# Optimization experiments

Measured on AMD Instinct MI355X. Metric: run time of the kernel, lower is better.

## Reference

```python
import jax, jax.numpy as jnp
import numpy as np

MO = 48          # max_output_len (positional slots)
D = 32           # d_inner
NA = 8           # n_actions
STOP = 0
CAT_PRIM, CAT_MOD, CAT_COMB = 0, 1, 2


def _mlp(feats, w1, b1, w2, b2, w3, b3):
    # Linear -> GELU(exact, erf) -> Linear -> GELU -> Linear (torch nn.GELU default is exact)
    h = jax.nn.gelu(feats @ w1.T + b1, approximate=False)
    h = jax.nn.gelu(h @ w2.T + b2, approximate=False)
    return h @ w3.T + b3


def setup_inputs() -> dict:
    key = jax.random.key(0)
    ks = jax.random.split(key, 20)
    B, N = 1024, 16
    inp = {
        'node_cats': jax.random.randint(ks[0], (B, N), 0, 3, dtype=jnp.int32),
        'node_subs': jax.random.randint(ks[1], (B, N), 0, 2, dtype=jnp.int32),
        'node_mask': jax.random.randint(ks[2], (B, N), 0, 2, dtype=jnp.int32),
        'child_left': jax.random.randint(ks[3], (B, N), 0, N, dtype=jnp.int32),
        'child_right': jax.random.randint(ks[4], (B, N), 0, N, dtype=jnp.int32),
        'action_embed': jax.random.normal(ks[5], (NA, D), jnp.float32),
        'mod_w1': jax.random.normal(ks[6], (128, 3), jnp.float32) * 0.1,
        'mod_b1': jax.random.normal(ks[7], (128,), jnp.float32) * 0.02,
        'mod_w2': jax.random.normal(ks[8], (128, 128), jnp.float32) * 0.05,
        'mod_b2': jax.random.normal(ks[9], (128,), jnp.float32) * 0.02,
        'mod_w3': jax.random.normal(ks[10], (MO * MO, 128), jnp.float32) * 0.01,
        'mod_b3': (4.0 * jnp.eye(MO)).flatten(),  # identity-ish init as in torch code
        'comb_w1': jax.random.normal(ks[11], (128, 4), jnp.float32) * 0.1,
        'comb_b1': jax.random.normal(ks[12], (128,), jnp.float32) * 0.02,
        'comb_w2': jax.random.normal(ks[13], (128, 128), jnp.float32) * 0.05,
        'comb_b2': jax.random.normal(ks[14], (128,), jnp.float32) * 0.02,
        'comb_w3': jax.random.normal(ks[15], (MO * 2 * MO, 128), jnp.float32) * 0.01,
        'comb_b3': (4.0 * jnp.eye(MO, 2 * MO)).flatten(),
    }
    return inp


def _forward(node_cats, node_subs, node_mask, child_left, child_right,
             action_embed, mod_w1, mod_b1, mod_w2, mod_b2, mod_w3, mod_b3,
             comb_w1, comb_b1, comb_w2, comb_b2, comb_w3, comb_b3):
    B, N = node_cats.shape
    mask = node_mask.astype(bool)
    cl = jnp.clip(child_left, 0, N - 1)
    cr = jnp.clip(child_right, 0, N - 1)
    prim_mask = (node_cats == CAT_PRIM) & mask
    mod_mask = (node_cats == CAT_MOD) & mask
    comb_mask = (node_cats == CAT_COMB) & mask
    subs01 = jnp.clip(node_subs, 0, 1)
    sub_oh = jax.nn.one_hot(subs01, 2, dtype=jnp.float32)  # (B,N,2)

    # --- primitive init: buffer[0] = action_embed[subs+1], zeros elsewhere ---
    action_ids = jnp.clip(node_subs + 1, 0, NA - 1)
    prim_vecs = action_embed[action_ids]  # (B,N,D)
    buffers = jnp.zeros((B, N, MO, D), jnp.float32)
    buffers = buffers.at[:, :, 0, :].set(prim_vecs * prim_mask[..., None].astype(jnp.float32))
    counts = prim_mask.astype(jnp.float32)  # (B,N)

    # --- modifier stage ---
    child_buf = jnp.take_along_axis(buffers, cl[:, :, None, None], axis=1)  # (B,N,MO,D)
    child_cnt = jnp.take_along_axis(counts, cl, axis=1)  # (B,N)
    feats = jnp.concatenate([child_cnt[..., None] / MO, sub_oh], axis=-1)  # (B,N,3)
    logits = _mlp(feats, mod_w1, mod_b1, mod_w2, mod_b2, mod_w3, mod_b3).reshape(B, N, MO, MO)
    attn = jax.nn.softmax(logits, axis=-1)
    mod_buf = jnp.einsum('bnpq,bnqd->bnpd', attn, child_buf)
    factors = jnp.array([2.0, 3.0], jnp.float32)[subs01]
    mod_cnt = jnp.minimum(child_cnt * factors, float(MO))
    buffers = jnp.where(mod_mask[:, :, None, None], mod_buf, buffers)
    counts = jnp.where(mod_mask, mod_cnt, counts)

    # --- combinator stage ---
    left_buf = jnp.take_along_axis(buffers, cl[:, :, None, None], axis=1)
    right_buf = jnp.take_along_axis(buffers, cr[:, :, None, None], axis=1)
    left_cnt = jnp.take_along_axis(counts, cl, axis=1)
    right_cnt = jnp.take_along_axis(counts, cr, axis=1)
    feats = jnp.concatenate([left_cnt[..., None] / MO, right_cnt[..., None] / MO, sub_oh], axis=-1)  # (B,N,4)
    logits = _mlp(feats, comb_w1, comb_b1, comb_w2, comb_b2, comb_w3, comb_b3).reshape(B, N, MO, 2 * MO)
    attn = jax.nn.softmax(logits, axis=-1)
    concat_buf = jnp.concatenate([left_buf, right_buf], axis=2)  # (B,N,2MO,D)
    comb_buf = jnp.einsum('bnpq,bnqd->bnpd', attn, concat_buf)
    comb_cnt = jnp.minimum(left_cnt + right_cnt, float(MO))
    buffers = jnp.where(comb_mask[:, :, None, None], comb_buf, buffers)
    counts = jnp.where(comb_mask, comb_cnt, counts)

    # --- decode root with tied embedding + stop bias ---
    root_buf = buffers[:, 0, :, :]  # (B,MO,D)
    out = jnp.einsum('bpd,ad->bpa', root_buf, action_embed)  # (B,MO,NA)
    positions = jnp.arange(MO, dtype=jnp.float32)[None, :]  # (1,MO)
    is_stop = (positions >= counts[:, 0:1]).astype(jnp.float32)[..., None]  # (B,MO,1)
    stop_bias = jnp.zeros((NA,), jnp.float32).at[STOP].set(8.0)
    return out + is_stop * stop_bias


def reference(node_cats, node_subs, node_mask, child_left, child_right,
              action_embed, mod_w1, mod_b1, mod_w2, mod_b2, mod_w3, mod_b3,
              comb_w1, comb_b1, comb_w2, comb_b2, comb_w3, comb_b3):
    return _forward(node_cats, node_subs, node_mask, child_left, child_right,
                    action_embed, mod_w1, mod_b1, mod_w2, mod_b2, mod_w3, mod_b3,
                    comb_w1, comb_b1, comb_w2, comb_b2, comb_w3, comb_b3)
```

## Files before the change

### kernel.cpp

```cpp
#include <hip/hip_runtime.h>
#include <hip/hip_bf16.h>
#include <float.h>


#define NNODE 16

#define MODCOL_OFF 0
#define C0_OFF     192
#define C48_OFF    1728
#define DOTL_OFF   3264
#define DOTR_OFF   9408
#define G_OFF      15552
#define H2_OFF     15616

__device__ __forceinline__ float gelu_exact(float x) {
    return 0.5f * x * (1.0f + erff(x * 0.70710678118654752f));
}

__device__ __forceinline__ float dot128(const float* __restrict__ w,
                                        const float* __restrict__ h) {
    const float4* w4 = (const float4*)w;
    float s = 0.f;
    #pragma unroll
    for (int i = 0; i < 32; ++i) {
        float4 v = w4[i];
        s += v.x * h[4 * i + 0] + v.y * h[4 * i + 1] +
             v.z * h[4 * i + 2] + v.w * h[4 * i + 3];
    }
    return s;
}

__global__ __launch_bounds__(128) void scan_tables_a(
    const float* __restrict__ E,
    const float* __restrict__ mw1, const float* __restrict__ mb1,
    const float* __restrict__ mw2, const float* __restrict__ mb2,
    const float* __restrict__ mw3, const float* __restrict__ mb3,
    const float* __restrict__ cw1, const float* __restrict__ cb1,
    const float* __restrict__ cw2, const float* __restrict__ cb2,
    float* __restrict__ ws)
{
    __shared__ float h1[128];
    __shared__ float h2s[128];
    __shared__ float lg[48];

    const int tid = threadIdx.x;
    const int blk = blockIdx.x;

    if (blk < 192) {
        const int m = blk / 48, p = blk % 48;
        const int cnt = m >> 1, sub = m & 1;
        const float f0 = (float)cnt / 48.0f;
        const float f1 = (sub == 0) ? 1.0f : 0.0f;
        const float f2 = (sub == 1) ? 1.0f : 0.0f;
        h1[tid] = gelu_exact(mw1[tid * 3 + 0] * f0 + mw1[tid * 3 + 1] * f1 +
                             mw1[tid * 3 + 2] * f2 + mb1[tid]);
        __syncthreads();
        h2s[tid] = gelu_exact(dot128(mw2 + tid * 128, h1) + mb2[tid]);
        __syncthreads();
        if (tid < 48)
            lg[tid] = dot128(mw3 + (p * 48 + tid) * 128, h2s) + mb3[p * 48 + tid];
        __syncthreads();
        if (tid == 0) {
            float mx = lg[0];
            for (int q = 1; q < 48; ++q) mx = fmaxf(mx, lg[q]);
            float s = 0.f;
            for (int q = 0; q < 48; ++q) s += expf(lg[q] - mx);
            ws[MODCOL_OFF + m * 48 + p] = expf(lg[0] - mx) / s;
        }
        return;
    }
    if (blk < 224) {
        const int c = blk - 192;
        const int csub = c & 1;
        const int rc = (c >> 1) & 3;
        const int lc = (c >> 3) & 3;
        const float f0 = (float)lc / 48.0f;
        const float f1 = (float)rc / 48.0f;
        const float f2 = (csub == 0) ? 1.0f : 0.0f;
        const float f3 = (csub == 1) ? 1.0f : 0.0f;
        h1[tid] = gelu_exact(cw1[tid * 4 + 0] * f0 + cw1[tid * 4 + 1] * f1 +
                             cw1[tid * 4 + 2] * f2 + cw1[tid * 4 + 3] * f3 + cb1[tid]);
        __syncthreads();
        ws[H2_OFF + c * 128 + tid] =
            gelu_exact(dot128(cw2 + tid * 128, h1) + cb2[tid]);
        return;
    }
    if (tid < 64) {
        const int i = tid >> 3, a = tid & 7;
        float s = 0.f;
        #pragma unroll
        for (int d = 0; d < 32; ++d) s += E[i * 32 + d] * E[a * 32 + d];
        ws[G_OFF + tid] = s;
    }
}

__global__ __launch_bounds__(128, 4) void scan_tables_b(
    const float* __restrict__ cw3, const float* __restrict__ cb3,
    float* __restrict__ ws)
{
    __shared__ float h2s[128];
    __shared__ float mc[192];
    __shared__ float lg[96];
    __shared__ float pr[96];
    __shared__ float red[4];

    const int tid = threadIdx.x;
    const int p = blockIdx.x >> 5;
    const int c = blockIdx.x & 31;

    h2s[tid] = ws[H2_OFF + c * 128 + tid];
    for (int i = tid; i < 192; i += 128) mc[i] = ws[MODCOL_OFF + i];
    __syncthreads();

    const int j = tid & 3;
    const int rbase = tid >> 2;
    const float4* h24 = (const float4*)h2s;
    #pragma unroll
    for (int o = 0; o < 3; ++o) {
        const int r = o * 32 + rbase;
        const float4* w4 = (const float4*)(cw3 + (p * 96 + r) * 128);
        float s = 0.f;
        #pragma unroll
        for (int i = 0; i < 8; ++i) {
            const int f4i = i * 4 + j;
            float4 w = w4[f4i];
            float4 h = h24[f4i];
            s += w.x * h.x + w.y * h.y + w.z * h.z + w.w * h.w;
        }
        s += __shfl_xor(s, 1);
        s += __shfl_xor(s, 2);
        if (j == 0) lg[r] = s;
    }
    __syncthreads();

    const int wv = tid >> 6;
    float lv = (tid < 96) ? (lg[tid] + cb3[p * 96 + tid]) : -FLT_MAX;
    float m = lv;
    #pragma unroll
    for (int d = 32; d > 0; d >>= 1) m = fmaxf(m, __shfl_xor(m, d));
    if ((tid & 63) == 0) red[wv] = m;
    __syncthreads();
    const float mx = fmaxf(red[0], red[1]);

    float ev = (tid < 96) ? expf(lv - mx) : 0.f;
    if (tid < 96) pr[tid] = ev;
    float sum = ev;
    #pragma unroll
    for (int d = 32; d > 0; d >>= 1) sum += __shfl_xor(sum, d);
    if ((tid & 63) == 0) red[2 + wv] = sum;
    __syncthreads();
    const float inv = 1.0f / (red[2] + red[3]);

    if (tid == 0) {
        ws[C0_OFF + c * 48 + p]  = pr[0]  * inv;
        ws[C48_OFF + c * 48 + p] = pr[48] * inv;
    }
    if (tid < 8) {
        const int mm = tid & 3;
        const int side = tid >> 2;
        const float* q0 = pr + side * 48;
        const float* mr = mc + mm * 48;
        float s = 0.f;
        #pragma unroll
        for (int q = 0; q < 48; ++q) s += q0[q] * mr[q];
        const int off = (side == 0 ? DOTL_OFF : DOTR_OFF) + (c * 4 + mm) * 48 + p;
        ws[off] = s * inv;
    }
}

__global__ __launch_bounds__(384) void scan_output(
    const int* __restrict__ cats, const int* __restrict__ subs,
    const int* __restrict__ mask, const int* __restrict__ cl,
    const int* __restrict__ cr,
    const float* __restrict__ ws,
    float* __restrict__ out)
{
    __shared__ int sc[NNODE], ss[NNODE], sm[NNODE], sl[NNODE], sr[NNODE];
    __shared__ int s_dec[7];
    __shared__ float s_G[64];

    const int b = blockIdx.x;
    const int tid = threadIdx.x;
    if (tid < NNODE) {
        sc[tid] = cats[b * NNODE + tid];
        ss[tid] = subs[b * NNODE + tid];
        sm[tid] = mask[b * NNODE + tid];
        sl[tid] = cl[b * NNODE + tid];
        sr[tid] = cr[b * NNODE + tid];
    } else if (tid >= 64 && tid < 128) {
        s_G[tid - 64] = ws[G_OFF + tid - 64];
    }
    __syncthreads();

    if (tid == 0) {
        auto clampN  = [](int x) { return x < 0 ? 0 : (x > NNODE - 1 ? NNODE - 1 : x); };
        auto clamp01 = [](int x) { return x < 0 ? 0 : (x > 1 ? 1 : x); };
        auto clampA  = [](int x) { return x < 0 ? 0 : (x > 7 ? 7 : x); };
        auto PRIM = [&](int n) { return (sc[n] == 0) && (sm[n] != 0); };
        auto MODM = [&](int n) { return (sc[n] == 1) && (sm[n] != 0); };
        auto AID  = [&](int n) { return clampA(ss[n] + 1); };

        int modeL = 0, modeR = 0, offL = 0, offR = 0, aidL = 0, aidR = 0, count0 = 0;
        const int  cat0 = sc[0];
        const bool msk0 = sm[0] != 0;
        const int  sub0 = clamp01(ss[0]);
        const int  cl0  = clampN(sl[0]);
        const int  cr0  = clampN(sr[0]);

        if (cat0 == 2 && msk0) {
            auto cnt2 = [&](int n) -> int {
                if (MODM(n)) {
                    int c1 = PRIM(clampN(sl[n])) ? 1 : 0;
                    int f  = clamp01(ss[n]) ? 3 : 2;
                    int v  = c1 * f;
                    return v > 48 ? 48 : v;
                }
                return PRIM(n) ? 1 : 0;
            };
            const int l = cl0, r = cr0;
            const int lcc = cnt2(l), rcc = cnt2(r);
            const int cidx = (lcc * 4 + rcc) * 2 + sub0;
            count0 = lcc + rcc; if (count0 > 48) count0 = 48;
            if (MODM(l)) {
                const int g = clampN(sl[l]);
                if (PRIM(g)) {
                    modeL = 1; aidL = AID(g);
                    const int mcfg = 2 + clamp01(ss[l]);
                    offL = DOTL_OFF + (cidx * 4 + mcfg) * 48;
                }
            } else if (PRIM(l)) {
                modeL = 1; aidL = AID(l);
                offL = C0_OFF + cidx * 48;
            }
            if (MODM(r)) {
                const int g = clampN(sl[r]);
                if (PRIM(g)) {
                    modeR = 1; aidR = AID(g);
                    const int mcfg = 2 + clamp01(ss[r]);
                    offR = DOTR_OFF + (cidx * 4 + mcfg) * 48;
                }
            } else if (PRIM(r)) {
                modeR = 1; aidR = AID(r);
                offR = C48_OFF + cidx * 48;
            }
        } else if (cat0 == 1 && msk0) {
            const int ch = cl0;
            const int c1 = PRIM(ch) ? 1 : 0;
            count0 = c1 * (sub0 ? 3 : 2); if (count0 > 48) count0 = 48;
            if (c1) {
                modeL = 1; aidL = AID(ch);
                offL = MODCOL_OFF + (2 + sub0) * 48;
            }
        } else if (cat0 == 0 && msk0) {
            modeL = 2; aidL = AID(0); count0 = 1;
        }
        s_dec[0] = modeL; s_dec[1] = modeR; s_dec[2] = offL; s_dec[3] = offR;
        s_dec[4] = aidL;  s_dec[5] = aidR;  s_dec[6] = count0;
    }
    __syncthreads();

    const int p = tid >> 3, a = tid & 7;
    const int modeL = s_dec[0], modeR = s_dec[1];
    float v = 0.f;
    if (modeL == 1)       v += ws[s_dec[2] + p] * s_G[s_dec[4] * 8 + a];
    else if (modeL == 2)  { if (p == 0) v = s_G[s_dec[4] * 8 + a]; }
    if (modeR == 1)       v += ws[s_dec[3] + p] * s_G[s_dec[5] * 8 + a];
    if (a == 0 && p >= s_dec[6]) v += 8.0f;
    out[b * 384 + tid] = v;
}

extern "C" void kernel_launch(void* const* d_in, const int* in_sizes, int n_in,
                              void* d_out, int out_size, void* d_ws, size_t ws_size,
                              hipStream_t stream) {
    const int* cats = (const int*)d_in[0];
    const int* subs = (const int*)d_in[1];
    const int* mask = (const int*)d_in[2];
    const int* cl   = (const int*)d_in[3];
    const int* cr   = (const int*)d_in[4];
    const float* E   = (const float*)d_in[5];
    const float* mw1 = (const float*)d_in[6];
    const float* mb1 = (const float*)d_in[7];
    const float* mw2 = (const float*)d_in[8];
    const float* mb2 = (const float*)d_in[9];
    const float* mw3 = (const float*)d_in[10];
    const float* mb3 = (const float*)d_in[11];
    const float* cw1 = (const float*)d_in[12];
    const float* cb1 = (const float*)d_in[13];
    const float* cw2 = (const float*)d_in[14];
    const float* cb2 = (const float*)d_in[15];
    const float* cw3 = (const float*)d_in[16];
    const float* cb3 = (const float*)d_in[17];
    float* ws  = (float*)d_ws;
    float* out = (float*)d_out;
    const int B = in_sizes[0] / NNODE;

    scan_tables_a<<<225, 128, 0, stream>>>(E, mw1, mb1, mw2, mb2, mw3, mb3,
                                           cw1, cb1, cw2, cb2, ws);
    scan_tables_b<<<48 * 32, 128, 0, stream>>>(cw3, cb3, ws);
    scan_output<<<B, 384, 0, stream>>>(cats, subs, mask, cl, cr, ws, out);
}
```

Measured before the change: 107.5 us.

## Merge table kernels into one launch and move mod-combine dot into output kernel

Fuses the two table-building kernels into a single launch. Each comb block now recomputes its own first two MLP layers instead of reading them from a prior kernel. Only the mod tables that are needed (count 1) are computed, and the full attention rows are stored to workspace. The mod-column dot product is deferred to the output kernel, which computes it per batch row from the stored attention. This removes one launch and an inter-kernel dependency, in exchange for redundant layer-2 MLP work in 1536 blocks and a larger workspace write plus per-row dot products in the output kernel.

```diff
diff --git a/kernel.cpp b/kernel.cpp
--- a/kernel.cpp
+++ b/kernel.cpp
@@ -6,12 +6,8 @@
 #define NNODE 16
 
 #define MODCOL_OFF 0
-#define C0_OFF     192
-#define C48_OFF    1728
-#define DOTL_OFF   3264
-#define DOTR_OFF   9408
-#define G_OFF      15552
-#define H2_OFF     15616
+#define G_OFF      192
+#define ATT_OFF    256
 
 __device__ __forceinline__ float gelu_exact(float x) {
     return 0.5f * x * (1.0f + erff(x * 0.70710678118654752f));
@@ -30,28 +26,29 @@
     return s;
 }
 
-__global__ __launch_bounds__(128) void scan_tables_a(
+__global__ __launch_bounds__(128) void scan_tables(
     const float* __restrict__ E,
     const float* __restrict__ mw1, const float* __restrict__ mb1,
     const float* __restrict__ mw2, const float* __restrict__ mb2,
     const float* __restrict__ mw3, const float* __restrict__ mb3,
     const float* __restrict__ cw1, const float* __restrict__ cb1,
     const float* __restrict__ cw2, const float* __restrict__ cb2,
+    const float* __restrict__ cw3, const float* __restrict__ cb3,
     float* __restrict__ ws)
 {
     __shared__ float h1[128];
     __shared__ float h2s[128];
-    __shared__ float lg[48];
+    __shared__ float lg[96];
+    __shared__ float red[4];
 
     const int tid = threadIdx.x;
     const int blk = blockIdx.x;
 
-    if (blk < 192) {
-        const int m = blk / 48, p = blk % 48;
-        const int cnt = m >> 1, sub = m & 1;
-        const float f0 = (float)cnt / 48.0f;
-        const float f1 = (sub == 0) ? 1.0f : 0.0f;
-        const float f2 = (sub == 1) ? 1.0f : 0.0f;
+    if (blk < 96) {
+        const int mm = blk / 48, p = blk % 48;
+        const float f0 = 1.0f / 48.0f;
+        const float f1 = (mm == 0) ? 1.0f : 0.0f;
+        const float f2 = (mm == 1) ? 1.0f : 0.0f;
         h1[tid] = gelu_exact(mw1[tid * 3 + 0] * f0 + mw1[tid * 3 + 1] * f1 +
                              mw1[tid * 3 + 2] * f2 + mb1[tid]);
         __syncthreads();
@@ -65,51 +62,36 @@
             for (int q = 1; q < 48; ++q) mx = fmaxf(mx, lg[q]);
             float s = 0.f;
             for (int q = 0; q < 48; ++q) s += expf(lg[q] - mx);
-            ws[MODCOL_OFF + m * 48 + p] = expf(lg[0] - mx) / s;
+            ws[MODCOL_OFF + (2 + mm) * 48 + p] = expf(lg[0] - mx) / s;
         }
         return;
     }
-    if (blk < 224) {
-        const int c = blk - 192;
-        const int csub = c & 1;
-        const int rc = (c >> 1) & 3;
-        const int lc = (c >> 3) & 3;
-        const float f0 = (float)lc / 48.0f;
-        const float f1 = (float)rc / 48.0f;
-        const float f2 = (csub == 0) ? 1.0f : 0.0f;
-        const float f3 = (csub == 1) ? 1.0f : 0.0f;
-        h1[tid] = gelu_exact(cw1[tid * 4 + 0] * f0 + cw1[tid * 4 + 1] * f1 +
-                             cw1[tid * 4 + 2] * f2 + cw1[tid * 4 + 3] * f3 + cb1[tid]);
-        __syncthreads();
-        ws[H2_OFF + c * 128 + tid] =
-            gelu_exact(dot128(cw2 + tid * 128, h1) + cb2[tid]);
+    if (blk == 96) {
+        if (tid < 64) {
+            const int i = tid >> 3, a = tid & 7;
+            float s = 0.f;
+            #pragma unroll
+            for (int d = 0; d < 32; ++d) s += E[i * 32 + d] * E[a * 32 + d];
+            ws[G_OFF + tid] = s;
+        }
         return;
     }
-    if (tid < 64) {
-        const int i = tid >> 3, a = tid & 7;
-        float s = 0.f;
-        #pragma unroll
-        for (int d = 0; d < 32; ++d) s += E[i * 32 + d] * E[a * 32 + d];
-        ws[G_OFF + tid] = s;
-    }
-}
-
-__global__ __launch_bounds__(128, 4) void scan_tables_b(
-    const float* __restrict__ cw3, const float* __restrict__ cb3,
-    float* __restrict__ ws)
-{
-    __shared__ float h2s[128];
-    __shared__ float mc[192];
-    __shared__ float lg[96];
-    __shared__ float pr[96];
-    __shared__ float red[4];
-
-    const int tid = threadIdx.x;
-    const int p = blockIdx.x >> 5;
-    const int c = blockIdx.x & 31;
-
-    h2s[tid] = ws[H2_OFF + c * 128 + tid];
-    for (int i = tid; i < 192; i += 128) mc[i] = ws[MODCOL_OFF + i];
+
+    const int u = blk - 97;
+    const int p = u >> 5;
+    const int c = u & 31;
+    const int csub = c & 1;
+    const int rc = (c >> 1) & 3;
+    const int lc = (c >> 3) & 3;
+
+    const float f0 = (float)lc / 48.0f;
+    const float f1 = (float)rc / 48.0f;
+    const float f2 = (csub == 0) ? 1.0f : 0.0f;
+    const float f3 = (csub == 1) ? 1.0f : 0.0f;
+    h1[tid] = gelu_exact(cw1[tid * 4 + 0] * f0 + cw1[tid * 4 + 1] * f1 +
+                         cw1[tid * 4 + 2] * f2 + cw1[tid * 4 + 3] * f3 + cb1[tid]);
+    __syncthreads();
+    h2s[tid] = gelu_exact(dot128(cw2 + tid * 128, h1) + cb2[tid]);
     __syncthreads();
 
     const int j = tid & 3;
@@ -143,7 +125,6 @@
     const float mx = fmaxf(red[0], red[1]);
 
     float ev = (tid < 96) ? expf(lv - mx) : 0.f;
-    if (tid < 96) pr[tid] = ev;
     float sum = ev;
     #pragma unroll
     for (int d = 32; d > 0; d >>= 1) sum += __shfl_xor(sum, d);
@@ -151,21 +132,8 @@
     __syncthreads();
     const float inv = 1.0f / (red[2] + red[3]);
 
-    if (tid == 0) {
-        ws[C0_OFF + c * 48 + p]  = pr[0]  * inv;
-        ws[C48_OFF + c * 48 + p] = pr[48] * inv;
-    }
-    if (tid < 8) {
-        const int mm = tid & 3;
-        const int side = tid >> 2;
-        const float* q0 = pr + side * 48;
-        const float* mr = mc + mm * 48;
-        float s = 0.f;
-        #pragma unroll
-        for (int q = 0; q < 48; ++q) s += q0[q] * mr[q];
-        const int off = (side == 0 ? DOTL_OFF : DOTR_OFF) + (c * 4 + mm) * 48 + p;
-        ws[off] = s * inv;
-    }
+    if (tid < 96)
+        ws[ATT_OFF + (c * 48 + p) * 96 + tid] = ev * inv;
 }
 
 __global__ __launch_bounds__(384) void scan_output(
@@ -176,8 +144,10 @@
     float* __restrict__ out)
 {
     __shared__ int sc[NNODE], ss[NNODE], sm[NNODE], sl[NNODE], sr[NNODE];
-    __shared__ int s_dec[7];
+    __shared__ int s_dec[11];
     __shared__ float s_G[64];
+    __shared__ float s_mc[96];
+    __shared__ float s_w[96];
 
     const int b = blockIdx.x;
     const int tid = threadIdx.x;
@@ -187,8 +157,10 @@
         sm[tid] = mask[b * NNODE + tid];
         sl[tid] = cl[b * NNODE + tid];
         sr[tid] = cr[b * NNODE + tid];
-    } else if (tid >= 64 && tid < 128) {
-        s_G[tid - 64] = ws[G_OFF + tid - 64];
+    } else if (tid >= 96 && tid < 192) {
+        s_mc[tid - 96] = ws[MODCOL_OFF + 96 + (tid - 96)];
+    } else if (tid >= 192 && tid < 256) {
+        s_G[tid - 192] = ws[G_OFF + tid - 192];
     }
     __syncthreads();
 
@@ -200,7 +172,8 @@
         auto MODM = [&](int n) { return (sc[n] == 1) && (sm[n] != 0); };
         auto AID  = [&](int n) { return clampA(ss[n] + 1); };
 
-        int modeL = 0, modeR = 0, offL = 0, offR = 0, aidL = 0, aidR = 0, count0 = 0;
+        int modeL = 0, modeR = 0, baseL = 0, baseR = 0, strideL = 0, strideR = 0;
+        int mselL = 0, mselR = 0, aidL = 0, aidR = 0, count0 = 0;
         const int  cat0 = sc[0];
         const bool msk0 = sm[0] != 0;
         const int  sub0 = clamp01(ss[0]);
@@ -220,28 +193,27 @@
             const int l = cl0, r = cr0;
             const int lcc = cnt2(l), rcc = cnt2(r);
             const int cidx = (lcc * 4 + rcc) * 2 + sub0;
+            const int abase = ATT_OFF + cidx * 4608;
             count0 = lcc + rcc; if (count0 > 48) count0 = 48;
             if (MODM(l)) {
                 const int g = clampN(sl[l]);
                 if (PRIM(g)) {
-                    modeL = 1; aidL = AID(g);
-                    const int mcfg = 2 + clamp01(ss[l]);
-                    offL = DOTL_OFF + (cidx * 4 + mcfg) * 48;
+                    modeL = 3; aidL = AID(g); mselL = clamp01(ss[l]);
+                    baseL = abase;
                 }
             } else if (PRIM(l)) {
                 modeL = 1; aidL = AID(l);
-                offL = C0_OFF + cidx * 48;
+                baseL = abase; strideL = 96;
             }
             if (MODM(r)) {
                 const int g = clampN(sl[r]);
                 if (PRIM(g)) {
-                    modeR = 1; aidR = AID(g);
-                    const int mcfg = 2 + clamp01(ss[r]);
-                    offR = DOTR_OFF + (cidx * 4 + mcfg) * 48;
+                    modeR = 3; aidR = AID(g); mselR = clamp01(ss[r]);
+                    baseR = abase + 48;
                 }
             } else if (PRIM(r)) {
                 modeR = 1; aidR = AID(r);
-                offR = C48_OFF + cidx * 48;
+                baseR = abase + 48; strideR = 96;
             }
         } else if (cat0 == 1 && msk0) {
             const int ch = cl0;
@@ -249,23 +221,49 @@
             count0 = c1 * (sub0 ? 3 : 2); if (count0 > 48) count0 = 48;
             if (c1) {
                 modeL = 1; aidL = AID(ch);
-                offL = MODCOL_OFF + (2 + sub0) * 48;
+                baseL = MODCOL_OFF + (2 + sub0) * 48; strideL = 1;
             }
         } else if (cat0 == 0 && msk0) {
             modeL = 2; aidL = AID(0); count0 = 1;
         }
-        s_dec[0] = modeL; s_dec[1] = modeR; s_dec[2] = offL; s_dec[3] = offR;
-        s_dec[4] = aidL;  s_dec[5] = aidR;  s_dec[6] = count0;
+        s_dec[0] = modeL;  s_dec[1] = modeR;
+        s_dec[2] = baseL;  s_dec[3] = baseR;
+        s_dec[4] = strideL; s_dec[5] = strideR;
+        s_dec[6] = mselL;  s_dec[7] = mselR;
+        s_dec[8] = aidL;   s_dec[9] = aidR;
+        s_dec[10] = count0;
+    }
+    __syncthreads();
+
+    if (tid < 96) {
+        const int side = tid / 48;
+        const int p = tid - side * 48;
+        const int mode = s_dec[0 + side];
+        const int base = s_dec[2 + side];
+        float w = 0.f;
+        if (mode == 1) {
+            w = ws[base + p * s_dec[4 + side]];
+        } else if (mode == 2) {
+            w = (p == 0) ? 1.0f : 0.0f;
+        } else if (mode == 3) {
+            const float4* ar = (const float4*)(ws + base + p * 96);
+            const float4* mr = (const float4*)(s_mc + s_dec[6 + side] * 48);
+            float s = 0.f;
+            #pragma unroll
+            for (int q = 0; q < 12; ++q) {
+                float4 a4 = ar[q], m4 = mr[q];
+                s += a4.x * m4.x + a4.y * m4.y + a4.z * m4.z + a4.w * m4.w;
+            }
+            w = s;
+        }
+        s_w[tid] = w;
     }
     __syncthreads();
 
     const int p = tid >> 3, a = tid & 7;
-    const int modeL = s_dec[0], modeR = s_dec[1];
-    float v = 0.f;
-    if (modeL == 1)       v += ws[s_dec[2] + p] * s_G[s_dec[4] * 8 + a];
-    else if (modeL == 2)  { if (p == 0) v = s_G[s_dec[4] * 8 + a]; }
-    if (modeR == 1)       v += ws[s_dec[3] + p] * s_G[s_dec[5] * 8 + a];
-    if (a == 0 && p >= s_dec[6]) v += 8.0f;
+    float v = s_w[p]      * s_G[s_dec[8] * 8 + a]
+            + s_w[48 + p] * s_G[s_dec[9] * 8 + a];
+    if (a == 0 && p >= s_dec[10]) v += 8.0f;
     out[b * 384 + tid] = v;
 }
 
@@ -294,8 +292,7 @@
     float* out = (float*)d_out;
     const int B = in_sizes[0] / NNODE;
 
-    scan_tables_a<<<225, 128, 0, stream>>>(E, mw1, mb1, mw2, mb2, mw3, mb3,
-                                           cw1, cb1, cw2, cb2, ws);
-    scan_tables_b<<<48 * 32, 128, 0, stream>>>(cw3, cb3, ws);
+    scan_tables<<<97 + 48 * 32, 128, 0, stream>>>(E, mw1, mb1, mw2, mb2, mw3, mb3,
+                                                  cw1, cb1, cw2, cb2, cw3, cb3, ws);
     scan_output<<<B, 384, 0, stream>>>(cats, subs, mask, cl, cr, ws, out);
 }
```

Result: slower. 113.1 us (+5.2%).
